# Optimization experiments

Measured on AMD Instinct MI355X. Metric: run time of the kernel, lower is better.

Reference implementation:

```python
import jax, jax.numpy as jnp
import numpy as np

B, N, C = 16, 4096, 768
H = 12
D = C // H  # 64
SCALE = D ** -0.5


def setup_inputs() -> dict:
    key = jax.random.key(0)
    k1, k2, k3, k4 = jax.random.split(key, 4)
    x = jax.random.normal(k1, (B, N, C), dtype=jnp.float32)
    # packed qkv projection (bias=False): torch Linear(dim, 3*dim)
    w_qkv = jax.random.normal(k2, (C, 3 * C), dtype=jnp.float32) * 0.02
    # output projection Linear(dim, dim) with bias
    w_proj = jax.random.normal(k3, (C, C), dtype=jnp.float32) * 0.02
    b_proj = jax.random.normal(k4, (C,), dtype=jnp.float32) * 0.02
    return {"x": x, "w_qkv": w_qkv, "w_proj": w_proj, "b_proj": b_proj}


def reference(x, w_qkv, w_proj, b_proj):
    b, n, c = x.shape
    # packed qkv: [B,N,3C] -> [3,B,H,N,D]
    qkv = (x @ w_qkv).reshape(b, n, 3, H, D).transpose(2, 0, 3, 1, 4)
    q, k, v = qkv[0], qkv[1], qkv[2]  # each [B,H,N,D]
    # kernelized (linear) attention: kv = (k^T v) * scale  -> [B,H,D,D]
    kv = jnp.einsum("bhnd,bhne->bhde", k, v) * SCALE
    # out = gelu(q) @ gelu(kv)  (exact/erf gelu, matching torch F.gelu default)
    gq = jax.nn.gelu(q, approximate=False)
    gkv = jax.nn.gelu(kv, approximate=False)
    out = jnp.einsum("bhtd,bhde->bhte", gq, gkv)  # [B,H,N,D]
    out = out.transpose(0, 2, 1, 3).reshape(b, n, c)  # b t (h d)
    return out @ w_proj + b_proj
```

## Files before the change

kernel.cpp:

```cpp
#include <hip/hip_runtime.h>
#include <hip/hip_bf16.h>


typedef __attribute__((ext_vector_type(8))) short short8_t;
typedef __attribute__((ext_vector_type(4))) float f32x4_t;

typedef __attribute__((address_space(1))) void as1_void;
typedef __attribute__((address_space(3))) void as3_void;

__device__ __forceinline__ void gload_lds16(const void* g, void* l) {
    __builtin_amdgcn_global_load_lds(
        (as1_void*)(unsigned long long)(g),
        (as3_void*)(unsigned long long)(l), 16, 0, 0);
}

__device__ __forceinline__ float gelu_f(float x) {
    float x2 = x * x;
    float t = x * fmaf(0.0356774081f, x2, 0.7978845608f);
    float e = __expf(2.0f * t);
    float th = 1.0f - 2.0f / (e + 1.0f);
    return 0.5f * x * (1.0f + th);
}

__device__ __forceinline__ unsigned short to_bf16(float f) {
    __hip_bfloat16 h = __float2bfloat16(f);
    return *reinterpret_cast<unsigned short*>(&h);
}

__device__ __forceinline__ f32x4_t mfma16(short8_t a, short8_t b, f32x4_t c) {
    return __builtin_amdgcn_mfma_f32_16x16x32_bf16(a, b, c, 0, 0, 0);
}

__global__ __launch_bounds__(256) void k_cvt_bf16(const float* __restrict__ in,
                                                  unsigned short* __restrict__ out,
                                                  long n) {
    long i = (long)blockIdx.x * blockDim.x + threadIdx.x;
    long stride = (long)gridDim.x * blockDim.x;
    for (long idx = i * 4; idx < n; idx += stride * 4) {
        float4 v = *(const float4*)(in + idx);
        ushort4 o;
        o.x = to_bf16(v.x); o.y = to_bf16(v.y); o.z = to_bf16(v.z); o.w = to_bf16(v.w);
        *(ushort4*)(out + idx) = o;
    }
}

__global__ __launch_bounds__(256) void k_wqkvT(const float* __restrict__ w,
                                               unsigned short* __restrict__ wT) {
    int gid = blockIdx.x * 256 + threadIdx.x;
    int c = gid / 96, rblk = gid % 96;
    int r0 = rblk * 8;
    short8_t o;
#pragma unroll
    for (int i = 0; i < 8; ++i)
        o[i] = (short)to_bf16(w[(size_t)(r0 + i) * 2304 + c]);
    *(short8_t*)(wT + (size_t)c * 768 + r0) = o;
}

__global__ __launch_bounds__(256) void k_wprojT(const float* __restrict__ w,
                                                unsigned short* __restrict__ wT) {
    int gid = blockIdx.x * 256 + threadIdx.x;
    int c = gid / 96, rblk = gid % 96;
    int r0 = rblk * 8;
    short8_t o;
#pragma unroll
    for (int i = 0; i < 8; ++i)
        o[i] = (short)to_bf16(w[(size_t)(r0 + i) * 768 + c]);
    *(short8_t*)(wT + (size_t)c * 768 + r0) = o;
}

template<bool GELU_EPI, bool BATCHED_B, bool BF16_OUT, bool BIAS>
__global__ __launch_bounds__(512, 2)
void k_gemm256(const unsigned short* __restrict__ A, int lda,
               const unsigned short* __restrict__ Bt, int ldb,
               void* __restrict__ Cout, int ldc,
               const float* __restrict__ bias,
               int tiles_n, int K) {
    __shared__ __attribute__((aligned(16))) unsigned short lds[2][2][2][128 * 64];

    const int nwg = gridDim.x;
    int bid = blockIdx.x;
    bid = (bid & 7) * (nwg >> 3) + (bid >> 3);

    const int tn = bid % tiles_n, tm = bid / tiles_n;
    const int row0 = tm * 256, col0 = tn * 256;

    const unsigned short* Bb = Bt;
    if (BATCHED_B) Bb += (size_t)(row0 >> 12) * 768 * 768;

    const int tid = threadIdx.x;
    const int lane = tid & 63;
    const int w = tid >> 6;
    const int wm = w >> 2;
    const int wn = w & 3;
    const int lr = lane & 15, lg = lane >> 4;

    const int c0 = tid, c1 = 512 + tid;
    const int sr0 = c0 >> 3, sk0 = (c0 & 7) ^ (sr0 & 7);
    const int sr1 = c1 >> 3, sk1 = (c1 & 7) ^ (sr1 & 7);

    auto stageA = [&](int buf, int half, int kt) {
        const unsigned short* base = A + (size_t)(row0 + half * 128) * lda + kt * 64;
        gload_lds16(base + (size_t)sr0 * lda + sk0 * 8, &lds[0][buf][half][c0 * 8]);
        gload_lds16(base + (size_t)sr1 * lda + sk1 * 8, &lds[0][buf][half][c1 * 8]);
    };
    auto stageB = [&](int buf, int half, int kt) {
        const unsigned short* base = Bb + (size_t)(col0 + half * 128) * ldb + kt * 64;
        gload_lds16(base + (size_t)sr0 * ldb + sk0 * 8, &lds[1][buf][half][c0 * 8]);
        gload_lds16(base + (size_t)sr1 * ldb + sk1 * 8, &lds[1][buf][half][c1 * 8]);
    };
    auto ldA = [&](int buf, int mi, int ks) -> short8_t {
        int row = mi * 16 + lr;
        int kc = (ks * 4 + lg) ^ (row & 7);
        return *(const short8_t*)&lds[0][buf][wm][row * 64 + kc * 8];
    };
    auto ldB = [&](int buf, int nj, int ks) -> short8_t {
        int row = wn * 64 + nj * 16 + lr;
        int half = row >> 7, rl = row & 127;
        int kc = (ks * 4 + lg) ^ (rl & 7);
        return *(const short8_t*)&lds[1][buf][half][rl * 64 + kc * 8];
    };

    f32x4_t acc[8][4] = {};
    short8_t bfrag[4][2];
    short8_t afrP[2][4];

#define FENCE asm volatile("" ::: "memory")
#define PH(q, STAGE_STMT, nbuf, nq)                                             \
    {                                                                           \
        asm volatile("s_waitcnt lgkmcnt(0)" ::: "memory");                      \
        __builtin_amdgcn_sched_barrier(0);                                      \
        __builtin_amdgcn_s_setprio(1);                                          \
        _Pragma("unroll") for (int nj = 0; nj < 4; ++nj) {                      \
            acc[2 * (q)][nj]     = mfma16(afrP[(q) & 1][0], bfrag[nj][0], acc[2 * (q)][nj]);     \
            acc[2 * (q)][nj]     = mfma16(afrP[(q) & 1][1], bfrag[nj][1], acc[2 * (q)][nj]);     \
            acc[2 * (q) + 1][nj] = mfma16(afrP[(q) & 1][2], bfrag[nj][0], acc[2 * (q) + 1][nj]); \
            acc[2 * (q) + 1][nj] = mfma16(afrP[(q) & 1][3], bfrag[nj][1], acc[2 * (q) + 1][nj]); \
        }                                                                       \
        __builtin_amdgcn_s_setprio(0);                                          \
        if ((q) == 3) {                                                         \
            _Pragma("unroll") for (int nj = 0; nj < 4; ++nj)                    \
                _Pragma("unroll") for (int ks = 0; ks < 2; ++ks)                \
                    bfrag[nj][ks] = ldB(nbuf, nj, ks);                          \
        }                                                                       \
        afrP[((q) + 1) & 1][0] = ldA(nbuf, 2 * (nq), 0);                        \
        afrP[((q) + 1) & 1][1] = ldA(nbuf, 2 * (nq), 1);                        \
        afrP[((q) + 1) & 1][2] = ldA(nbuf, 2 * (nq) + 1, 0);                    \
        afrP[((q) + 1) & 1][3] = ldA(nbuf, 2 * (nq) + 1, 1);                    \
        STAGE_STMT;                                                             \
        asm volatile("s_waitcnt vmcnt(2)" ::: "memory");                        \
        FENCE;                                                                  \
        __builtin_amdgcn_s_barrier();                                           \
        FENCE;                                                                  \
    }

    const int nt = K >> 6;
    const int niter = nt >> 1;

    stageA(0, 0, 0); stageA(0, 1, 0); stageB(0, 0, 0); stageB(0, 1, 0);
    asm volatile("s_waitcnt vmcnt(0)" ::: "memory");
    stageB(1, 0, 1); stageB(1, 1, 1); stageA(1, 0, 1);
    __builtin_amdgcn_s_barrier();
    FENCE;
#pragma unroll
    for (int nj = 0; nj < 4; ++nj)
#pragma unroll
        for (int ks = 0; ks < 2; ++ks)
            bfrag[nj][ks] = ldB(0, nj, ks);
    afrP[0][0] = ldA(0, 0, 0); afrP[0][1] = ldA(0, 0, 1);
    afrP[0][2] = ldA(0, 1, 0); afrP[0][3] = ldA(0, 1, 1);
    FENCE;

    for (int it = 0; it < niter; ++it) {
        const int t1 = 2 * it + 1;
        const int tA = (2 * it + 2 < nt) ? 2 * it + 2 : 0;
        const int tB = (2 * it + 3 < nt) ? 2 * it + 3 : 0;
        PH(0, stageA(1, 1, t1), 0, 1);
        PH(1, stageB(0, 0, tA), 0, 2);
        PH(2, stageB(0, 1, tA), 0, 3);
        PH(3, stageA(0, 0, tA), 1, 0);
        PH(0, stageA(0, 1, tA), 1, 1);
        PH(1, stageB(1, 0, tB), 1, 2);
        PH(2, stageB(1, 1, tB), 1, 3);
        PH(3, stageA(1, 0, tB), 0, 0);
    }
    asm volatile("s_waitcnt vmcnt(0)" ::: "memory");
#undef PH
#undef FENCE

    const int rbase = row0 + wm * 128 + (lg << 2);
    const int cbase = col0 + wn * 64 + lr;
#pragma unroll
    for (int mi = 0; mi < 8; ++mi)
#pragma unroll
        for (int nj = 0; nj < 4; ++nj)
#pragma unroll
            for (int r = 0; r < 4; ++r) {
                int row = rbase + mi * 16 + r;
                int col = cbase + nj * 16;
                float v = acc[mi][nj][r];
                if (GELU_EPI) v = gelu_f(v);
                if (BIAS) v += bias[col];
                if (BF16_OUT)
                    ((unsigned short*)Cout)[(size_t)row * ldc + col] = to_bf16(v);
                else
                    ((float*)Cout)[(size_t)row * ldc + col] = v;
            }
}

__global__ __launch_bounds__(256) void k_G(const unsigned short* __restrict__ xb,
                                           unsigned short* __restrict__ Gst) {
    static const signed char TI[21] = {0,0,0,0,0,0,1,1,1,1,1,2,2,2,2,3,3,3,4,4,5};
    static const signed char TJ[21] = {0,1,2,3,4,5,1,2,3,4,5,2,3,4,5,3,4,5,4,5,5};
    int bid = blockIdx.x;
    bid = (bid & 7) * 42 + (bid >> 3);
    const int b = bid / 21, t = bid % 21;
    const int d0 = TI[t] * 128, e0 = TJ[t] * 128;
    const bool diag = (d0 == e0);
    const unsigned short* xB = xb + (size_t)b * 4096 * 768;

    __shared__ __attribute__((aligned(16))) unsigned short lds[2][2][128 * 64];

    const int tid = threadIdx.x, lane = tid & 63, w = tid >> 6;
    const int colg = tid & 15;
    const int rq8 = (tid >> 4) & 7;
    const int blk = tid >> 7;
    const int wm = w >> 1, wn = w & 1;
    const int lr = lane & 15, lg = lane >> 4;
    const int base0 = (blk ? e0 : d0) + colg * 8;
    const int tb = diag ? 0 : 1;
    const bool active = (!diag) || (blk == 0);

    f32x4_t acc[4][4] = {};
    short8_t ra[8];

    auto loadx = [&](int it) {
        if (!active) return;
        const size_t rbase = (size_t)(it * 64 + rq8 * 8) * 768 + base0;
#pragma unroll
        for (int rr = 0; rr < 8; ++rr)
            ra[rr] = *(const short8_t*)(xB + rbase + (size_t)rr * 768);
    };
    auto writes = [&](int buf) {
        if (!active) return;
#pragma unroll
        for (int j = 0; j < 8; ++j) {
            const int c = colg * 8 + j;
            const int sw3 = ((c & 7) ^ (c >> 3)) & 7;
            short8_t v;
#pragma unroll
            for (int rr = 0; rr < 8; ++rr) v[rr] = ra[rr][j];
            *(short8_t*)(&lds[buf][blk][c * 64 + ((rq8 ^ sw3) << 3)]) = v;
        }
    };
    auto ldfrag = [&](int buf, int tile, int cbase, int o) -> short8_t {
        const int c = cbase + lr;
        const int sw3 = ((c & 7) ^ (c >> 3)) & 7;
        return *(const short8_t*)(&lds[buf][tile][c * 64 + ((o ^ sw3) << 3)]);
    };

    loadx(0);
    writes(0);
    __syncthreads();

    for (int it = 0; it < 64; ++it) {
        const int buf = it & 1;
        if (it < 63) loadx(it + 1);
#pragma unroll
        for (int ks = 0; ks < 2; ++ks) {
            short8_t af[4], bf[4];
#pragma unroll
            for (int mi = 0; mi < 4; ++mi)
                af[mi] = ldfrag(buf, 0, wm * 64 + mi * 16, ks * 4 + lg);
#pragma unroll
            for (int nj = 0; nj < 4; ++nj)
                bf[nj] = ldfrag(buf, tb, wn * 64 + nj * 16, ks * 4 + lg);
#pragma unroll
            for (int mi = 0; mi < 4; ++mi)
#pragma unroll
                for (int nj = 0; nj < 4; ++nj)
                    acc[mi][nj] = mfma16(af[mi], bf[nj], acc[mi][nj]);
        }
        if (it < 63) writes(buf ^ 1);
        __syncthreads();
    }

    const int dbase = d0 + wm * 64 + (lg << 2);
    const int ebase = e0 + wn * 64 + lr;
#pragma unroll
    for (int mi = 0; mi < 4; ++mi)
#pragma unroll
        for (int nj = 0; nj < 4; ++nj)
#pragma unroll
            for (int r = 0; r < 4; ++r)
                Gst[((size_t)b * 768 + dbase + mi * 16 + r) * 768 + ebase + nj * 16] =
                    to_bf16(acc[mi][nj][r]);

    if (!diag) {
        unsigned short* T = &lds[0][0][0];
#pragma unroll
        for (int mi = 0; mi < 4; ++mi)
#pragma unroll
            for (int nj = 0; nj < 4; ++nj) {
                const int el = wn * 64 + nj * 16 + lr;
                const int sig = ((el ^ (el >> 3)) & 7) << 1;
                const int s = wm * 16 + mi * 4 + lg;
                uint2 pk;
                pk.x = (unsigned int)to_bf16(acc[mi][nj][0]) |
                       ((unsigned int)to_bf16(acc[mi][nj][1]) << 16);
                pk.y = (unsigned int)to_bf16(acc[mi][nj][2]) |
                       ((unsigned int)to_bf16(acc[mi][nj][3]) << 16);
                *(uint2*)(&T[el * 128 + ((s ^ sig) << 2)]) = pk;
            }
        __syncthreads();
#pragma unroll
        for (int i = 0; i < 8; ++i) {
            const int el = i * 16 + (tid >> 4);
            const int p = tid & 15;
            const int sig = ((el ^ (el >> 3)) & 7) << 1;
            short8_t v = *(const short8_t*)(&T[el * 128 + (((2 * p) ^ sig) << 2)]);
            *(short8_t*)(Gst + ((size_t)b * 768 + e0 + el) * 768 + d0 + p * 8) = v;
        }
    }
}

__global__ __launch_bounds__(256) void k_kvh(const unsigned short* __restrict__ wqkv_bf,
                                             const unsigned short* __restrict__ Tst,
                                             unsigned short* __restrict__ gkvb) {
    const int bh = blockIdx.x;
    const int b = bh / 12, h = bh % 12;
    const unsigned short* kptr = wqkv_bf + 768 + h * 64;
    const unsigned short* vptr = Tst + (size_t)b * 768 * 768 + h * 64;

    __shared__ __attribute__((aligned(16))) unsigned short kT[64 * 64];
    __shared__ __attribute__((aligned(16))) unsigned short vT[64 * 64];

    const int tid = threadIdx.x, lane = tid & 63, w = tid >> 6;
    const int np = tid >> 3;
    const int g = tid & 7;

    f32x4_t acc[4] = {};

    for (int it = 0; it < 12; ++it) {
        const size_t r = (size_t)(it * 64 + 2 * np);
        short8_t k0 = *(const short8_t*)(kptr + r * 2304 + g * 8);
        short8_t k1 = *(const short8_t*)(kptr + (r + 1) * 2304 + g * 8);
        short8_t v0 = *(const short8_t*)(vptr + r * 768 + g * 8);
        short8_t v1 = *(const short8_t*)(vptr + (r + 1) * 768 + g * 8);
        __syncthreads();
#pragma unroll
        for (int j = 0; j < 8; ++j) {
            const int d = g * 8 + j;
            const int e = d * 64 + ((2 * np) ^ (((d ^ (d >> 3)) & 7) << 3));
            *(unsigned int*)(kT + e) =
                (unsigned int)(unsigned short)k0[j] | ((unsigned int)(unsigned short)k1[j] << 16);
            *(unsigned int*)(vT + e) =
                (unsigned int)(unsigned short)v0[j] | ((unsigned int)(unsigned short)v1[j] << 16);
        }
        __syncthreads();
        const int lr = lane & 15, lg = lane >> 4;
#pragma unroll
        for (int ks = 0; ks < 2; ++ks) {
            const int d = w * 16 + lr;
            short8_t a = *(const short8_t*)(kT + d * 64 +
                (((ks * 4 + lg) ^ ((d ^ (d >> 3)) & 7)) << 3));
#pragma unroll
            for (int nj = 0; nj < 4; ++nj) {
                const int e2 = nj * 16 + lr;
                short8_t bf = *(const short8_t*)(vT + e2 * 64 +
                    (((ks * 4 + lg) ^ ((e2 ^ (e2 >> 3)) & 7)) << 3));
                acc[nj] = __builtin_amdgcn_mfma_f32_16x16x32_bf16(a, bf, acc[nj], 0, 0, 0);
            }
        }
    }

    unsigned short* pout = gkvb + (size_t)bh * 4096;
    const int rb2 = w * 16 + ((lane >> 4) << 2);
    const int cb = lane & 15;
#pragma unroll
    for (int nj = 0; nj < 4; ++nj)
#pragma unroll
        for (int r = 0; r < 4; ++r)
            pout[(rb2 + r) * 64 + nj * 16 + cb] = to_bf16(gelu_f(acc[nj][r] * 0.125f));
}

__global__ __launch_bounds__(256) void k_M(const unsigned short* __restrict__ gkvb,
                                           const unsigned short* __restrict__ wpT,
                                           unsigned short* __restrict__ MT) {
    __shared__ __attribute__((aligned(16))) unsigned short As[64 * 64];
    __shared__ __attribute__((aligned(16))) unsigned short Bs[256 * 64];

    const int bid = blockIdx.x;
    const int bh = bid / 3, ct = bid % 3;
    const int b = bh / 12, h = bh % 12;
    const int c0 = ct * 256;
    const int tid = threadIdx.x, lane = tid & 63, w = tid >> 6;
    const int lr = lane & 15, lg = lane >> 4;

    short8_t ra[2], rb[8];
#pragma unroll
    for (int i = 0; i < 2; ++i) {
        int ch = i * 256 + tid, row = ch >> 3, kc = ch & 7;
        ra[i] = *(const short8_t*)(gkvb + (size_t)bh * 4096 + row * 64 + kc * 8);
    }
#pragma unroll
    for (int i = 0; i < 8; ++i) {
        int ch = i * 256 + tid, row = ch >> 3, kc = ch & 7;
        rb[i] = *(const short8_t*)(wpT + (size_t)(c0 + row) * 768 + h * 64 + kc * 8);
    }
#pragma unroll
    for (int i = 0; i < 2; ++i) {
        int ch = i * 256 + tid, row = ch >> 3, kc = ch & 7;
        *(short8_t*)(As + row * 64 + ((kc ^ (row & 7)) * 8)) = ra[i];
    }
#pragma unroll
    for (int i = 0; i < 8; ++i) {
        int ch = i * 256 + tid, row = ch >> 3, kc = ch & 7;
        *(short8_t*)(Bs + row * 64 + ((kc ^ (row & 7)) * 8)) = rb[i];
    }
    __syncthreads();

    f32x4_t acc[4][4] = {};
#pragma unroll
    for (int ks = 0; ks < 2; ++ks) {
        short8_t a[4], bfr[4];
#pragma unroll
        for (int mi = 0; mi < 4; ++mi) {
            int row = mi * 16 + lr;
            a[mi] = *(const short8_t*)(As + row * 64 + (((ks * 4 + lg) ^ (row & 7)) * 8));
        }
#pragma unroll
        for (int nj = 0; nj < 4; ++nj) {
            int row = w * 64 + nj * 16 + lr;
            bfr[nj] = *(const short8_t*)(Bs + row * 64 + (((ks * 4 + lg) ^ (row & 7)) * 8));
        }
#pragma unroll
        for (int mi = 0; mi < 4; ++mi)
#pragma unroll
            for (int nj = 0; nj < 4; ++nj)
                acc[mi][nj] = __builtin_amdgcn_mfma_f32_16x16x32_bf16(a[mi], bfr[nj], acc[mi][nj], 0, 0, 0);
    }
    __syncthreads();

#pragma unroll
    for (int mi = 0; mi < 4; ++mi)
#pragma unroll
        for (int nj = 0; nj < 4; ++nj) {
            unsigned int w0 = (unsigned int)to_bf16(acc[mi][nj][0]) |
                              ((unsigned int)to_bf16(acc[mi][nj][1]) << 16);
            unsigned int w1 = (unsigned int)to_bf16(acc[mi][nj][2]) |
                              ((unsigned int)to_bf16(acc[mi][nj][3]) << 16);
            uint2 pk; pk.x = w0; pk.y = w1;
            *(uint2*)(Bs + (w * 64 + nj * 16 + lr) * 64 + mi * 16 + lg * 4) = pk;
        }
    __syncthreads();
#pragma unroll
    for (int i = 0; i < 8; ++i) {
        int ch = i * 256 + tid, cl = ch >> 3, dk = ch & 7;
        short8_t v = *(const short8_t*)(Bs + cl * 64 + dk * 8);
        *(short8_t*)(MT + ((size_t)(b * 768) + c0 + cl) * 768 + h * 64 + dk * 8) = v;
    }
}

extern "C" void kernel_launch(void* const* d_in, const int* in_sizes, int n_in,
                              void* d_out, int out_size, void* d_ws, size_t ws_size,
                              hipStream_t stream) {
    const float* x      = (const float*)d_in[0];
    const float* w_qkv  = (const float*)d_in[1];
    const float* w_proj = (const float*)d_in[2];
    const float* b_proj = (const float*)d_in[3];
    float* out = (float*)d_out;
    char* ws = (char*)d_ws;

    unsigned short* q_gelu  = (unsigned short*)(ws);
    unsigned short* wqkvT   = (unsigned short*)(ws + 100663296);
    unsigned short* wqkv_bf = (unsigned short*)(ws + 104202240);
    unsigned short* G_bf    = (unsigned short*)(ws + 107741184);
    unsigned short* T_bf    = (unsigned short*)(ws + 126615552);
    unsigned short* MT      = (unsigned short*)(ws + 145489920);
    unsigned short* xb   = (unsigned short*)d_out;
    unsigned short* gkvb = (unsigned short*)((char*)d_out + 134217728);
    unsigned short* wpT  = (unsigned short*)((char*)d_out + 136314880);

    k_cvt_bf16<<<2048, 256, 0, stream>>>(x, xb, 50331648L);
    k_cvt_bf16<<<432, 256, 0, stream>>>(w_qkv, wqkv_bf, 1769472L);
    k_wqkvT<<<864, 256, 0, stream>>>(w_qkv, wqkvT);
    k_wprojT<<<288, 256, 0, stream>>>(w_proj, wpT);
    k_gemm256<true, false, true, false><<<768, 512, 0, stream>>>(
        xb, 768, wqkvT, 768, q_gelu, 768, nullptr, 3, 768);
    k_G<<<336, 256, 0, stream>>>(xb, G_bf);
    k_gemm256<false, false, true, false><<<144, 512, 0, stream>>>(
        G_bf, 768, wqkvT + (size_t)1536 * 768, 768, T_bf, 768, nullptr, 3, 768);
    k_kvh<<<192, 256, 0, stream>>>(wqkv_bf, T_bf, gkvb);
    k_M<<<576, 256, 0, stream>>>(gkvb, wpT, MT);
    k_gemm256<false, true, false, true><<<768, 512, 0, stream>>>(
        q_gelu, 768, MT, 768, out, 768, b_proj, 3, 768);
}
```

Before: 414.3 us.

## Restructure GEMM main loop into per-tile groups with partial LDS waits

Replaces the eight-phase pipeline macro with a per-K-tile GROUP that issues A-fragment LDS reads ahead and waits only partially (lgkmcnt(4)) before each MFMA cluster. Global-to-LDS staging is reordered so B halves are staged mid-group and both A halves at the end, with the vmcnt thresholds changed to match. The prologue now stages the whole second tile. The aim is to overlap LDS reads with MFMA work and relax barrier stalls. It risks races on the double-buffered LDS if the new wait counts or barrier placement are wrong.

```diff
diff --git a/kernel.cpp b/kernel.cpp
--- a/kernel.cpp
+++ b/kernel.cpp
@@ -125,32 +125,53 @@
     short8_t afrP[2][4];
 
 #define FENCE asm volatile("" ::: "memory")
-#define PH(q, STAGE_STMT, nbuf, nq)                                             \
-    {                                                                           \
-        asm volatile("s_waitcnt lgkmcnt(0)" ::: "memory");                      \
-        __builtin_amdgcn_sched_barrier(0);                                      \
-        __builtin_amdgcn_s_setprio(1);                                          \
-        _Pragma("unroll") for (int nj = 0; nj < 4; ++nj) {                      \
-            acc[2 * (q)][nj]     = mfma16(afrP[(q) & 1][0], bfrag[nj][0], acc[2 * (q)][nj]);     \
-            acc[2 * (q)][nj]     = mfma16(afrP[(q) & 1][1], bfrag[nj][1], acc[2 * (q)][nj]);     \
-            acc[2 * (q) + 1][nj] = mfma16(afrP[(q) & 1][2], bfrag[nj][0], acc[2 * (q) + 1][nj]); \
-            acc[2 * (q) + 1][nj] = mfma16(afrP[(q) & 1][3], bfrag[nj][1], acc[2 * (q) + 1][nj]); \
-        }                                                                       \
-        __builtin_amdgcn_s_setprio(0);                                          \
-        if ((q) == 3) {                                                         \
-            _Pragma("unroll") for (int nj = 0; nj < 4; ++nj)                    \
-                _Pragma("unroll") for (int ks = 0; ks < 2; ++ks)                \
-                    bfrag[nj][ks] = ldB(nbuf, nj, ks);                          \
-        }                                                                       \
-        afrP[((q) + 1) & 1][0] = ldA(nbuf, 2 * (nq), 0);                        \
-        afrP[((q) + 1) & 1][1] = ldA(nbuf, 2 * (nq), 1);                        \
-        afrP[((q) + 1) & 1][2] = ldA(nbuf, 2 * (nq) + 1, 0);                    \
-        afrP[((q) + 1) & 1][3] = ldA(nbuf, 2 * (nq) + 1, 1);                    \
-        STAGE_STMT;                                                             \
-        asm volatile("s_waitcnt vmcnt(2)" ::: "memory");                        \
-        FENCE;                                                                  \
-        __builtin_amdgcn_s_barrier();                                           \
-        FENCE;                                                                  \
+#define MFMACL(r0i, par)                                                        \
+    __builtin_amdgcn_s_setprio(1);                                              \
+    _Pragma("unroll") for (int nj = 0; nj < 4; ++nj) {                          \
+        acc[r0i][nj]     = mfma16(afrP[par][0], bfrag[nj][0], acc[r0i][nj]);    \
+        acc[r0i][nj]     = mfma16(afrP[par][1], bfrag[nj][1], acc[r0i][nj]);    \
+        acc[r0i + 1][nj] = mfma16(afrP[par][2], bfrag[nj][0], acc[r0i + 1][nj]);\
+        acc[r0i + 1][nj] = mfma16(afrP[par][3], bfrag[nj][1], acc[r0i + 1][nj]);\
+    }                                                                           \
+    __builtin_amdgcn_s_setprio(0);
+
+#define GROUP(cb, nb, tnx)                                                      \
+    {                                 \
+      afrP[0][0] = ldA(cb, 0, 0); afrP[0][1] = ldA(cb, 0, 1);                   \
+      afrP[0][2] = ldA(cb, 1, 0); afrP[0][3] = ldA(cb, 1, 1);                   \
+      afrP[1][0] = ldA(cb, 2, 0); afrP[1][1] = ldA(cb, 2, 1);                   \
+      afrP[1][2] = ldA(cb, 3, 0); afrP[1][3] = ldA(cb, 3, 1);                   \
+      asm volatile("s_waitcnt lgkmcnt(4)" ::: "memory");                        \
+      __builtin_amdgcn_sched_barrier(0);                                        \
+      MFMACL(0, 0)                                                              \
+      stageB(cb, 0, tnx);                                                       \
+      FENCE; __builtin_amdgcn_s_barrier(); FENCE;                               \
+                                              \
+      afrP[0][0] = ldA(cb, 4, 0); afrP[0][1] = ldA(cb, 4, 1);                   \
+      afrP[0][2] = ldA(cb, 5, 0); afrP[0][3] = ldA(cb, 5, 1);                   \
+      asm volatile("s_waitcnt lgkmcnt(4)" ::: "memory");                        \
+      __builtin_amdgcn_sched_barrier(0);                                        \
+      MFMACL(2, 1)                                                              \
+      stageB(cb, 1, tnx);                                                       \
+      FENCE; __builtin_amdgcn_s_barrier(); FENCE;                               \
+                                              \
+      afrP[1][0] = ldA(cb, 6, 0); afrP[1][1] = ldA(cb, 6, 1);                   \
+      afrP[1][2] = ldA(cb, 7, 0); afrP[1][3] = ldA(cb, 7, 1);                   \
+      asm volatile("s_waitcnt lgkmcnt(4)" ::: "memory");                        \
+      __builtin_amdgcn_sched_barrier(0);                                        \
+      MFMACL(4, 0)                                                              \
+      asm volatile("s_waitcnt vmcnt(8)" ::: "memory");                          \
+      FENCE; __builtin_amdgcn_s_barrier(); FENCE;                               \
+       \
+      asm volatile("s_waitcnt lgkmcnt(0)" ::: "memory");                        \
+      __builtin_amdgcn_sched_barrier(0);                                        \
+      MFMACL(6, 1)                                                              \
+      _Pragma("unroll") for (int nj = 0; nj < 4; ++nj)                          \
+          _Pragma("unroll") for (int ks = 0; ks < 2; ++ks)                      \
+              bfrag[nj][ks] = ldB(nb, nj, ks);                                  \
+      stageA(cb, 0, tnx); stageA(cb, 1, tnx);                                   \
+      asm volatile("s_waitcnt vmcnt(8)" ::: "memory");                          \
+      FENCE; __builtin_amdgcn_s_barrier(); FENCE;                               \
     }
 
     const int nt = K >> 6;
@@ -158,33 +179,26 @@
 
     stageA(0, 0, 0); stageA(0, 1, 0); stageB(0, 0, 0); stageB(0, 1, 0);
     asm volatile("s_waitcnt vmcnt(0)" ::: "memory");
-    stageB(1, 0, 1); stageB(1, 1, 1); stageA(1, 0, 1);
     __builtin_amdgcn_s_barrier();
     FENCE;
+    stageB(1, 0, 1); stageB(1, 1, 1); stageA(1, 0, 1); stageA(1, 1, 1);
 #pragma unroll
     for (int nj = 0; nj < 4; ++nj)
 #pragma unroll
         for (int ks = 0; ks < 2; ++ks)
             bfrag[nj][ks] = ldB(0, nj, ks);
-    afrP[0][0] = ldA(0, 0, 0); afrP[0][1] = ldA(0, 0, 1);
-    afrP[0][2] = ldA(0, 1, 0); afrP[0][3] = ldA(0, 1, 1);
+    asm volatile("s_waitcnt lgkmcnt(0)" ::: "memory");
     FENCE;
 
     for (int it = 0; it < niter; ++it) {
-        const int t1 = 2 * it + 1;
         const int tA = (2 * it + 2 < nt) ? 2 * it + 2 : 0;
         const int tB = (2 * it + 3 < nt) ? 2 * it + 3 : 0;
-        PH(0, stageA(1, 1, t1), 0, 1);
-        PH(1, stageB(0, 0, tA), 0, 2);
-        PH(2, stageB(0, 1, tA), 0, 3);
-        PH(3, stageA(0, 0, tA), 1, 0);
-        PH(0, stageA(0, 1, tA), 1, 1);
-        PH(1, stageB(1, 0, tB), 1, 2);
-        PH(2, stageB(1, 1, tB), 1, 3);
-        PH(3, stageA(1, 0, tB), 0, 0);
+        GROUP(0, 1, tA);
+        GROUP(1, 0, tB);
     }
     asm volatile("s_waitcnt vmcnt(0)" ::: "memory");
-#undef PH
+#undef GROUP
+#undef MFMACL
 #undef FENCE
 
     const int rbase = row0 + wm * 128 + (lg << 2);
```

Result: faster. 394.8 us (-4.7%).
